# Kernel optimization log

Measured on AMD Instinct MI355X. Metric: run time of the kernel, lower is better.

The kernel has to match this reference:

```python
import jax, jax.numpy as jnp
import numpy as np

NUM_USERS = 100000
NUM_ITEMS = 20000
DIM = 64
NUM_TAG = 64
NUM_NEG = 8
B = 262144
M_IMP = 2000
MARGIN1 = 0.1
MARGIN2 = 0.1
LAMBDA1 = 1.0
LAMBDA2 = 1.0
TAU = 0.2
EPS = 1e-7
MAX_NORM = 1.0 - 1e-5


def _norm(x, keepdims=True):
    return jnp.sqrt(jnp.maximum(jnp.sum(x * x, -1, keepdims=keepdims), 1e-15))


def artanh(x):
    x = jnp.clip(x, -MAX_NORM, MAX_NORM)
    return 0.5 * (jnp.log1p(x) - jnp.log1p(-x))


def acosh(z):
    z = jnp.maximum(z, 1.0 + EPS)
    return jnp.log(z + jnp.sqrt(z * z - 1.0))


# ---- Poincare ball, c = 1 ----
def ball_projx(x):
    n = _norm(x)
    return jnp.where(n > MAX_NORM, x * (MAX_NORM / n), x)


def ball_expmap0(u):
    n = _norm(u)
    return jnp.tanh(n) * u / n


def ball_logmap0(x):
    n = _norm(x)
    return artanh(n) * x / n


def mobius_add(x, y):
    xy = jnp.sum(x * y, -1, keepdims=True)
    x2 = jnp.sum(x * x, -1, keepdims=True)
    y2 = jnp.sum(y * y, -1, keepdims=True)
    num = (1.0 + 2.0 * xy + y2) * x + (1.0 - x2) * y
    den = 1.0 + 2.0 * xy + x2 * y2
    return num / jnp.maximum(den, 1e-15)


def mobius_matvec(w, x):
    # x: [..., in], w: [out, in] -> mx = x @ w.T (geoopt convention)
    mx = x @ w.T
    xn = _norm(x)
    mn = _norm(mx)
    return jnp.tanh(mn / xn * artanh(xn)) * mx / mn


def ball_dist2(x, y):
    d = 2.0 * artanh(_norm(mobius_add(-x, y), keepdims=False))
    return d * d


# ---- Lorentz, k = 1 ----
def lorentz_dist2(x, y):
    inner = jnp.sum(x[..., 1:] * y[..., 1:], -1) - x[..., 0] * y[..., 0]
    d = acosh(-inner)
    return d * d


def setup_inputs() -> dict:
    key = jax.random.key(0)
    ks = jax.random.split(key, 10)
    # Lorentz points (k=1): x0 = sqrt(1 + ||x_spatial||^2)
    sp = jax.random.normal(ks[0], (NUM_USERS + NUM_ITEMS, DIM - 1), jnp.float32) * 0.5
    t = jnp.sqrt(1.0 + jnp.sum(sp * sp, -1, keepdims=True))
    embeddings = jnp.concatenate([t, sp], -1)
    vtg_weight = jax.random.normal(ks[1], (NUM_ITEMS, DIM), jnp.float32) * 0.01
    emb_tag = ball_expmap0(jax.random.normal(ks[2], (NUM_TAG, DIM), jnp.float32) * 0.1)
    kk = (6.0 / (2 * DIM)) ** 0.5
    lin_weight = jax.random.uniform(ks[3], (DIM, DIM), jnp.float32, -kk, kk)
    lin_bias = ball_expmap0(jax.random.normal(ks[4], (DIM,), jnp.float32) * 0.001)
    tag_weight = jnp.zeros((NUM_TAG,), jnp.float32)
    uu = jax.random.randint(ks[5], (B, 1), 0, NUM_USERS)
    it = jax.random.randint(ks[6], (B, 1 + NUM_NEG), NUM_USERS, NUM_USERS + NUM_ITEMS)
    triples = jnp.concatenate([uu, it], 1)
    tag_labels = jax.random.randint(ks[7], (NUM_ITEMS, NUM_TAG), 0, 2)
    a = jax.random.randint(ks[8], (M_IMP,), 0, NUM_TAG)
    b = (a + 1 + jax.random.randint(ks[9], (M_IMP,), 0, NUM_TAG - 1)) % NUM_TAG
    implication = jnp.stack([a, b], 1)
    return dict(embeddings=embeddings, vtg_weight=vtg_weight, emb_tag=emb_tag,
                lin_weight=lin_weight, lin_bias=lin_bias, tag_weight=tag_weight,
                triples=triples, tag_labels=tag_labels, implication=implication)


def reference(embeddings, vtg_weight, emb_tag, lin_weight, lin_bias, tag_weight,
              triples, tag_labels, implication):
    # ---- hyperbolic margin-ranking loss ----
    u = embeddings[triples[:, 0]]                         # [B, D]
    pos = embeddings[triples[:, 1]]                       # [B, D]
    neg = embeddings[triples[:, 2:]]                      # [B, NEG, D]
    pos_scores = lorentz_dist2(u, pos)[:, None]           # [B, 1]
    neg_scores = lorentz_dist2(u[:, None, :], neg)        # [B, NEG]
    # alpha = sqrt(dist2(u, origin)) = acosh(u0) for Lorentz k=1
    alpha = acosh(u[:, 0])[:, None]
    rank_loss = jnp.sum(jnp.maximum((pos_scores - neg_scores + MARGIN2) * alpha, 0.0))

    # ---- Ex_loss: MobiusLinear then tangent-space cdist ----
    enc = ball_projx(vtg_weight)
    h = mobius_matvec(lin_weight, enc)
    h = ball_projx(mobius_add(h, lin_bias[None, :]))
    a = ball_logmap0(h)                                   # [I, D]
    bt = ball_logmap0(emb_tag)                            # [T, D]
    sq = jnp.sum(a * a, -1)[:, None] + jnp.sum(bt * bt, -1)[None, :] - 2.0 * a @ bt.T
    dist = jnp.sqrt(jnp.maximum(sq, 1e-12))
    logits = dist / jnp.exp(tag_weight)[None, :]          # [I, T]
    logp = jnp.log(logits)
    # relu(log(target) - log(all_dist) + margin1) summed over all tags,
    # masked to the positive-tag positions (== np.where(tag_labels>0) gather)
    term = jnp.maximum(logp[:, :, None] - logp[:, None, :] + MARGIN1, 0.0)  # [I, T, T]
    mask = (tag_labels > 0).astype(logp.dtype)
    cls_loss = jnp.sum(term.sum(-1) * mask)

    # ---- tag-hierarchy contrastive loss ----
    q = emb_tag[implication[:, 0]]
    p = emb_tag[implication[:, 1]]
    dist_pos = ball_dist2(q, p)[:, None]                               # [M, 1]
    dist_neg = ball_dist2(q[:, None, :], emb_tag[None, :, :])          # [M, T]
    full = jnp.concatenate([dist_pos, dist_neg], 1)                    # [M, T+1]
    # original filters out entries <= 1e-9 (the self-distance zero); masking
    # them to -inf in logit space is the permutation-invariant equivalent
    cl_logits = jnp.where(full > 1e-9, -full / TAU, -1e30)
    cl_loss = jnp.sum(jax.nn.logsumexp(cl_logits, axis=1) + dist_pos[:, 0] / TAU)

    return rank_loss + LAMBDA1 * cls_loss + LAMBDA2 * cl_loss
```

## Files before the change

### kernel.cpp

```cpp
#include <hip/hip_runtime.h>
#include <math.h>

namespace {

constexpr int NUM_NEG   = 8;
constexpr int BROWS     = 262144;
constexpr int NUM_ITEMS_C = 20000;
constexpr int M_IMP_C   = 2000;
constexpr float MARGIN1 = 0.1f;
constexpr float MARGIN2 = 0.1f;
constexpr float TAU     = 0.2f;
constexpr float EPS1    = 1e-7f;
constexpr float MAXNORM = 1.0f - 1e-5f;

constexpr int NBLK   = 4096;
constexpr int NWAVES = NBLK * 4;

__device__ __forceinline__ float wredsum(float v) {
    v += __shfl_xor(v, 1);  v += __shfl_xor(v, 2);  v += __shfl_xor(v, 4);
    v += __shfl_xor(v, 8);  v += __shfl_xor(v, 16); v += __shfl_xor(v, 32);
    return v;
}
__device__ __forceinline__ float wredmax(float v) {
    v = fmaxf(v, __shfl_xor(v, 1));  v = fmaxf(v, __shfl_xor(v, 2));
    v = fmaxf(v, __shfl_xor(v, 4));  v = fmaxf(v, __shfl_xor(v, 8));
    v = fmaxf(v, __shfl_xor(v, 16)); v = fmaxf(v, __shfl_xor(v, 32));
    return v;
}
__device__ __forceinline__ float bcast(float v, int l) {
    return __int_as_float(__builtin_amdgcn_readlane(__float_as_int(v), l));
}
__device__ __forceinline__ float fsq(float x)  { return __builtin_amdgcn_sqrtf(x); }
__device__ __forceinline__ float frc(float x)  { return __builtin_amdgcn_rcpf(x); }
__device__ __forceinline__ float artanh_fast(float n) {
    n = fminf(n, MAXNORM);
    return 0.5f * __logf((1.f + n) * frc(1.f - n));
}
__device__ __forceinline__ float acosh_fast(float z) {
    z = fmaxf(z, 1.0f + EPS1);
    return __logf(z + fsq(fmaf(z, z, -1.0f)));
}
__device__ __forceinline__ float tanh_fast(float x) {
    const float t = __expf(2.f * x);
    return (t - 1.f) * frc(t + 1.f);
}
__device__ __forceinline__ float dot4(const float4& a, const float4& b) {
    return (a.x * b.x + a.y * b.y) + (a.z * b.z + a.w * b.w);
}

__global__ __launch_bounds__(256) void fused_kernel(
        const float* __restrict__ emb,  const int* __restrict__ tri,
        const float* __restrict__ vtg,  const float* __restrict__ etag,
        const float* __restrict__ linw, const float* __restrict__ linb,
        const float* __restrict__ tw,   const int* __restrict__ labels,
        const int* __restrict__ imp,    float* __restrict__ part) {
    __shared__ float SA[64 * 65];
    __shared__ float s64[64];
    __shared__ float red4[4];
    const int tid  = threadIdx.x;
    const int lane = tid & 63, wid = tid >> 6;
    const int b    = blockIdx.x;
    const int gw   = b * 4 + wid;
    float wacc = 0.f;

    for (int i = tid; i < 4096; i += 256) {
        const int r = i >> 6, d = i & 63;
        SA[d * 65 + r] = linw[i];
    }
    __syncthreads();
    const float bias = linb[lane];
    const float y2b  = wredsum(bias * bias);
    const int i0 = gw, i1 = gw + NWAVES;
    const bool v1 = (i1 < NUM_ITEMS_C);

    float xv0 = vtg[(long)i0 * 64 + lane];
    float xv1 = v1 ? vtg[(long)i1 * 64 + lane] : 0.f;

    auto prep = [&](float& x) -> float {
        float n2 = wredsum(x * x);
        float n  = fsq(fmaxf(n2, 1e-15f));
        if (n > MAXNORM) {
            x *= MAXNORM * frc(n);
            n2 = wredsum(x * x);
            n  = fsq(fmaxf(n2, 1e-15f));
        }
        return n;
    };
    const float xn0 = prep(xv0);
    const float xn1 = prep(xv1);

    float ma0 = 0.f, ma1 = 0.f, mb0 = 0.f, mb1 = 0.f;
    #pragma unroll
    for (int d = 0; d < 64; d += 2) {
        const float w0 = SA[(d)     * 65 + lane];
        const float w1 = SA[(d + 1) * 65 + lane];
        ma0 = fmaf(bcast(xv0, d), w0, ma0);  ma1 = fmaf(bcast(xv0, d + 1), w1, ma1);
        mb0 = fmaf(bcast(xv1, d), w0, mb0);  mb1 = fmaf(bcast(xv1, d + 1), w1, mb1);
    }
    auto tail = [&](float mx, float xn) -> float {
        const float mn  = fsq(fmaxf(wredsum(mx * mx), 1e-15f));
        const float g   = tanh_fast(mn * frc(xn) * artanh_fast(xn));
        const float h1  = g * frc(mn) * mx;
        const float x2h = wredsum(h1 * h1);
        const float xy  = wredsum(h1 * bias);
        const float A   = 1.f + 2.f * xy + y2b;
        const float Bc  = 1.f - x2h;
        const float den = fmaxf(1.f + 2.f * xy + x2h * y2b, 1e-15f);
        float hh = (A * h1 + Bc * bias) * frc(den);
        float hn = fsq(fmaxf(wredsum(hh * hh), 1e-15f));
        if (hn > MAXNORM) {
            hh *= MAXNORM * frc(hn);
            hn = fsq(fmaxf(wredsum(hh * hh), 1e-15f));
        }
        return artanh_fast(hn) * frc(hn) * hh;
    };
    const float av0 = tail(ma0 + ma1, xn0);
    const float av1 = tail(mb0 + mb1, xn1);
    __syncthreads();
    {
        const int j = tid >> 2, p = tid & 3;
        float e[16]; float s2 = 0.f;
        #pragma unroll
        for (int m = 0; m < 16; ++m) { e[m] = etag[j * 64 + p * 16 + m]; s2 += e[m] * e[m]; }
        s2 += __shfl_xor(s2, 1); s2 += __shfl_xor(s2, 2);
        const float n  = fsq(fmaxf(s2, 1e-15f));
        const float sc = artanh_fast(n) * frc(n);
        #pragma unroll
        for (int m = 0; m < 16; ++m) SA[(p * 16 + m) * 65 + j] = sc * e[m];
        if (p == 0) s64[j] = sc * sc * s2;
    }
    __syncthreads();
    const float twl = tw[lane];
    const float b2l = s64[lane];
    float da0 = 0.f, da1 = 0.f, db0 = 0.f, db1 = 0.f;
    #pragma unroll
    for (int d = 0; d < 64; d += 2) {
        const float w0 = SA[(d)     * 65 + lane];
        const float w1 = SA[(d + 1) * 65 + lane];
        da0 = fmaf(bcast(av0, d), w0, da0);  da1 = fmaf(bcast(av0, d + 1), w1, da1);
        db0 = fmaf(bcast(av1, d), w0, db0);  db1 = fmaf(bcast(av1, d + 1), w1, db1);
    }
    auto hinge = [&](float a, float dot, int i) -> float {
        const float a2v  = wredsum(a * a);
        const float dist = fsq(fmaxf(a2v + b2l - 2.f * dot, 1e-12f));
        const float logp = __logf(dist) - twl;
        float s0 = 0.f, s1 = 0.f, s2 = 0.f, s3 = 0.f;
        #pragma unroll
        for (int k = 0; k < 64; k += 4) {
            s0 += fmaxf(logp - bcast(logp, k)     + MARGIN1, 0.f);
            s1 += fmaxf(logp - bcast(logp, k + 1) + MARGIN1, 0.f);
            s2 += fmaxf(logp - bcast(logp, k + 2) + MARGIN1, 0.f);
            s3 += fmaxf(logp - bcast(logp, k + 3) + MARGIN1, 0.f);
        }
        const float hs = (s0 + s1) + (s2 + s3);
        const float c  = (labels[(long)i * 64 + lane] > 0) ? hs : 0.f;
        return wredsum(c);
    };
    wacc += hinge(av0, da0 + da1, i0);
    if (v1) wacc += hinge(av1, db0 + db1, i1);
    __syncthreads();

    {
        const int j = tid >> 2, p = tid & 3;
        float s2 = 0.f;
        #pragma unroll
        for (int m = 0; m < 16; ++m) {
            const float e = etag[j * 64 + p * 16 + m];
            s2 += e * e;
            SA[(p * 16 + m) * 65 + j] = e;
        }
        s2 += __shfl_xor(s2, 1); s2 += __shfl_xor(s2, 2);
        if (p == 0) s64[j] = s2;
    }
    __syncthreads();
    if (gw < M_IMP_C) {
        const int ai = imp[gw * 2];
        const int bi = imp[gw * 2 + 1];
        const float y2l = s64[lane];
        const float x2  = s64[ai];
        float c0 = 0.f, c1 = 0.f, c2 = 0.f, c3 = 0.f;
        #pragma unroll
        for (int d = 0; d < 64; d += 4) {
            c0 = fmaf(SA[(d)     * 65 + ai], SA[(d)     * 65 + lane], c0);
            c1 = fmaf(SA[(d + 1) * 65 + ai], SA[(d + 1) * 65 + lane], c1);
            c2 = fmaf(SA[(d + 2) * 65 + ai], SA[(d + 2) * 65 + lane], c2);
            c3 = fmaf(SA[(d + 3) * 65 + ai], SA[(d + 3) * 65 + lane], c3);
        }
        const float c   = (c0 + c1) + (c2 + c3);
        const float A   = 1.f - 2.f * c + y2l;
        const float Bc  = 1.f - x2;
        const float nn  = A * A * x2 - 2.f * A * Bc * c + Bc * Bc * y2l;
        const float den = fmaxf(1.f - 2.f * c + x2 * y2l, 1e-15f);
        float n = fsq(fmaxf(nn * frc(den * den), 1e-15f));
        n = fminf(n, MAXNORM);
        const float dd = __logf((1.f + n) * frc(1.f - n));
        float dist = dd * dd;
        if (lane == ai) dist = 0.f;
        const float logit = (dist > 1e-9f) ? (-dist * (1.f / TAU)) : -1e30f;
        const float dp = bcast(dist, bi);
        const float lp = bcast(logit, bi);
        const float m  = wredmax(logit);
        const float se = wredsum(__expf(logit - m)) + __expf(lp - m);
        wacc += m + __logf(se) + dp * (1.f / TAU);
    }

    {
        const int sub = lane & 7;
        const int rw  = lane >> 3;
        const int dof = sub * 8;
        const bool o0 = sub & 1;
        const bool o1 = (sub >> 1) & 1;
        const bool o2 = (sub >> 2) & 1;
        float racc = 0.f;

        const int  row0 = gw * 8 + rw;
        const int* t0 = tri + (long)row0 * 10;
        const int* t1 = t0 + (long)(NWAVES * 8) * 10;
        const int2 a01 = *reinterpret_cast<const int2*>(t0);
        const int2 a23 = *reinterpret_cast<const int2*>(t0 + 2);
        const int2 a45 = *reinterpret_cast<const int2*>(t0 + 4);
        const int2 a67 = *reinterpret_cast<const int2*>(t0 + 6);
        const int2 a89 = *reinterpret_cast<const int2*>(t0 + 8);
        const int2 b01 = *reinterpret_cast<const int2*>(t1);
        const int2 b23 = *reinterpret_cast<const int2*>(t1 + 2);
        const int2 b45 = *reinterpret_cast<const int2*>(t1 + 4);
        const int2 b67 = *reinterpret_cast<const int2*>(t1 + 6);
        const int2 b89 = *reinterpret_cast<const int2*>(t1 + 8);

        auto ldvec = [&](int idx, float4& lo, float4& hi) {
            const float* q = emb + (long)idx * 64 + dof;
            lo = *reinterpret_cast<const float4*>(q);
            hi = *reinterpret_cast<const float4*>(q + 4);
        };
        auto finish = [&](float e0, float e1, float e2, float e3,
                          float e4, float e5, float e6, float e7,
                          float ps, float alpha) {
            float s_;
            s_ = o0 ? e0 : e1; s_ = __shfl_xor(s_, 1); const float f0 = (o0 ? e1 : e0) + s_;
            s_ = o0 ? e2 : e3; s_ = __shfl_xor(s_, 1); const float f1 = (o0 ? e3 : e2) + s_;
            s_ = o0 ? e4 : e5; s_ = __shfl_xor(s_, 1); const float f2 = (o0 ? e5 : e4) + s_;
            s_ = o0 ? e6 : e7; s_ = __shfl_xor(s_, 1); const float f3 = (o0 ? e7 : e6) + s_;
            s_ = o1 ? f0 : f1; s_ = __shfl_xor(s_, 2); const float g0 = (o1 ? f1 : f0) + s_;
            s_ = o1 ? f2 : f3; s_ = __shfl_xor(s_, 2); const float g1 = (o1 ? f3 : f2) + s_;
            s_ = o2 ? g0 : g1; s_ = __shfl_xor(s_, 4); const float dn = (o2 ? g1 : g0) + s_;
            const float dneg = acosh_fast(-dn);
            float hk = fmaxf(ps - dneg * dneg + MARGIN2, 0.f);
            hk += __shfl_xor(hk, 1); hk += __shfl_xor(hk, 2); hk += __shfl_xor(hk, 4);
            if (sub == 0) racc += alpha * hk;
        };

        float4 ua0, ub0, pa0, pb0, ua1, ub1, pa1, pb1;
        ldvec(a01.x, ua0, ub0);  ldvec(a01.y, pa0, pb0);
        ldvec(b01.x, ua1, ub1);  ldvec(b01.y, pa1, pb1);

        float4 na0,nb0, na1,nb1, na2,nb2, na3,nb3, na4,nb4, na5,nb5, na6,nb6, na7,nb7;
        ldvec(a23.x, na0, nb0);  ldvec(a23.y, na1, nb1);
        ldvec(a45.x, na2, nb2);  ldvec(a45.y, na3, nb3);
        ldvec(a67.x, na4, nb4);  ldvec(a67.y, na5, nb5);
        ldvec(a89.x, na6, nb6);  ldvec(a89.y, na7, nb7);

        const float u00 = ua0.x;
        if (sub == 0) ua0.x = -ua0.x;
        float dp0 = dot4(ua0, pa0) + dot4(ub0, pb0);
        dp0 += __shfl_xor(dp0, 1); dp0 += __shfl_xor(dp0, 2); dp0 += __shfl_xor(dp0, 4);
        const float dpos0  = acosh_fast(-dp0);
        const float ps0    = dpos0 * dpos0;
        const float alpha0 = acosh_fast(u00);
        const float e0 = dot4(ua0, na0) + dot4(ub0, nb0);
        const float e1 = dot4(ua0, na1) + dot4(ub0, nb1);
        const float e2 = dot4(ua0, na2) + dot4(ub0, nb2);
        const float e3 = dot4(ua0, na3) + dot4(ub0, nb3);
        const float e4 = dot4(ua0, na4) + dot4(ub0, nb4);
        const float e5 = dot4(ua0, na5) + dot4(ub0, nb5);
        const float e6 = dot4(ua0, na6) + dot4(ub0, nb6);
        const float e7 = dot4(ua0, na7) + dot4(ub0, nb7);

        float4 ma0v,mb0v, ma1v,mb1v, ma2v,mb2v, ma3v,mb3v,
               ma4v,mb4v, ma5v,mb5v, ma6v,mb6v, ma7v,mb7v;
        ldvec(b23.x, ma0v, mb0v);  ldvec(b23.y, ma1v, mb1v);
        ldvec(b45.x, ma2v, mb2v);  ldvec(b45.y, ma3v, mb3v);
        ldvec(b67.x, ma4v, mb4v);  ldvec(b67.y, ma5v, mb5v);
        ldvec(b89.x, ma6v, mb6v);  ldvec(b89.y, ma7v, mb7v);

        finish(e0, e1, e2, e3, e4, e5, e6, e7, ps0, alpha0);

        const float u01 = ua1.x;
        if (sub == 0) ua1.x = -ua1.x;
        float dp1 = dot4(ua1, pa1) + dot4(ub1, pb1);
        dp1 += __shfl_xor(dp1, 1); dp1 += __shfl_xor(dp1, 2); dp1 += __shfl_xor(dp1, 4);
        const float dpos1  = acosh_fast(-dp1);
        const float ps1    = dpos1 * dpos1;
        const float alpha1 = acosh_fast(u01);
        const float h0 = dot4(ua1, ma0v) + dot4(ub1, mb0v);
        const float h1 = dot4(ua1, ma1v) + dot4(ub1, mb1v);
        const float h2 = dot4(ua1, ma2v) + dot4(ub1, mb2v);
        const float h3 = dot4(ua1, ma3v) + dot4(ub1, mb3v);
        const float h4 = dot4(ua1, ma4v) + dot4(ub1, mb4v);
        const float h5 = dot4(ua1, ma5v) + dot4(ub1, mb5v);
        const float h6 = dot4(ua1, ma6v) + dot4(ub1, mb6v);
        const float h7 = dot4(ua1, ma7v) + dot4(ub1, mb7v);
        finish(h0, h1, h2, h3, h4, h5, h6, h7, ps1, alpha1);

        wacc += wredsum(racc);
    }

    if (lane == 0) red4[wid] = wacc;
    __syncthreads();
    if (tid == 0) part[b] = red4[0] + red4[1] + red4[2] + red4[3];
}

__global__ __launch_bounds__(256) void final_reduce(
        const float* __restrict__ parts, int n, float* __restrict__ out) {
    __shared__ double red[256];
    double s = 0.0;
    for (int i = threadIdx.x; i < n; i += 256) s += (double)parts[i];
    red[threadIdx.x] = s;
    __syncthreads();
    for (int off = 128; off > 0; off >>= 1) {
        if (threadIdx.x < off) red[threadIdx.x] += red[threadIdx.x + off];
        __syncthreads();
    }
    if (threadIdx.x == 0) out[0] = (float)red[0];
}

}

extern "C" void kernel_launch(void* const* d_in, const int* in_sizes, int n_in,
                              void* d_out, int out_size, void* d_ws, size_t ws_size,
                              hipStream_t stream) {
    const float* emb    = (const float*)d_in[0];
    const float* vtg    = (const float*)d_in[1];
    const float* etag   = (const float*)d_in[2];
    const float* linw   = (const float*)d_in[3];
    const float* linb   = (const float*)d_in[4];
    const float* tw     = (const float*)d_in[5];
    const int*   tri    = (const int*)d_in[6];
    const int*   labels = (const int*)d_in[7];
    const int*   imp    = (const int*)d_in[8];
    float* parts = (float*)d_ws;

    fused_kernel<<<NBLK, 256, 0, stream>>>(emb, tri, vtg, etag, linw, linb,
                                           tw, labels, imp, parts);
    final_reduce<<<1, 256, 0, stream>>>(parts, NBLK, (float*)d_out);
}
```

Baseline: 84.06 us.

## Split fused loss kernel into separate rank, classification and contrastive kernels

The single fused kernel, where every block staged the linear weights and tag tables in shared memory and ran all three loss parts, is split into three kernels. Each kernel is sized to its own work: 4096 blocks for ranking, 2500 for classification (two items per wave, no bounds checks) and 500 for the contrastive loss. The ranking blocks no longer pay for the shared-memory setup and extra syncs of the other parts. The classification path now broadcasts through LDS instead of readlane and batches independent wave reductions. The cost is two extra kernel launches and the loss of overlap between the memory-bound ranking work and the compute-bound classification work.

```diff
diff --git a/kernel.cpp b/kernel.cpp
--- a/kernel.cpp
+++ b/kernel.cpp
@@ -5,7 +5,6 @@
 
 constexpr int NUM_NEG   = 8;
 constexpr int BROWS     = 262144;
-constexpr int NUM_ITEMS_C = 20000;
 constexpr int M_IMP_C   = 2000;
 constexpr float MARGIN1 = 0.1f;
 constexpr float MARGIN2 = 0.1f;
@@ -13,13 +12,39 @@
 constexpr float EPS1    = 1e-7f;
 constexpr float MAXNORM = 1.0f - 1e-5f;
 
-constexpr int NBLK   = 4096;
-constexpr int NWAVES = NBLK * 4;
+constexpr int RANK_BLOCKS = 4096;
+constexpr int RANK_WAVES  = RANK_BLOCKS * 4;
+constexpr int CLS_BLOCKS  = 2500;
+constexpr int CLS_WAVES   = CLS_BLOCKS * 4;
+constexpr int CL_BLOCKS   = 500;
+constexpr int NPART = RANK_BLOCKS + CLS_BLOCKS + CL_BLOCKS;
 
 __device__ __forceinline__ float wredsum(float v) {
     v += __shfl_xor(v, 1);  v += __shfl_xor(v, 2);  v += __shfl_xor(v, 4);
     v += __shfl_xor(v, 8);  v += __shfl_xor(v, 16); v += __shfl_xor(v, 32);
     return v;
+}
+__device__ __forceinline__ void wredsum2(float& a, float& b) {
+    a += __shfl_xor(a, 1);  b += __shfl_xor(b, 1);
+    a += __shfl_xor(a, 2);  b += __shfl_xor(b, 2);
+    a += __shfl_xor(a, 4);  b += __shfl_xor(b, 4);
+    a += __shfl_xor(a, 8);  b += __shfl_xor(b, 8);
+    a += __shfl_xor(a, 16); b += __shfl_xor(b, 16);
+    a += __shfl_xor(a, 32); b += __shfl_xor(b, 32);
+}
+__device__ __forceinline__ void wredsum4(float& a, float& b, float& c, float& d) {
+    a += __shfl_xor(a, 1);  b += __shfl_xor(b, 1);
+    c += __shfl_xor(c, 1);  d += __shfl_xor(d, 1);
+    a += __shfl_xor(a, 2);  b += __shfl_xor(b, 2);
+    c += __shfl_xor(c, 2);  d += __shfl_xor(d, 2);
+    a += __shfl_xor(a, 4);  b += __shfl_xor(b, 4);
+    c += __shfl_xor(c, 4);  d += __shfl_xor(d, 4);
+    a += __shfl_xor(a, 8);  b += __shfl_xor(b, 8);
+    c += __shfl_xor(c, 8);  d += __shfl_xor(d, 8);
+    a += __shfl_xor(a, 16); b += __shfl_xor(b, 16);
+    c += __shfl_xor(c, 16); d += __shfl_xor(d, 16);
+    a += __shfl_xor(a, 32); b += __shfl_xor(b, 32);
+    c += __shfl_xor(c, 32); d += __shfl_xor(d, 32);
 }
 __device__ __forceinline__ float wredmax(float v) {
     v = fmaxf(v, __shfl_xor(v, 1));  v = fmaxf(v, __shfl_xor(v, 2));
@@ -48,74 +73,183 @@
     return (a.x * b.x + a.y * b.y) + (a.z * b.z + a.w * b.w);
 }
 
-__global__ __launch_bounds__(256) void fused_kernel(
-        const float* __restrict__ emb,  const int* __restrict__ tri,
+__global__ __launch_bounds__(256) void rank_kernel(
+        const float* __restrict__ emb, const int* __restrict__ tri,
+        float* __restrict__ part) {
+    __shared__ float red4[4];
+    const int tid  = threadIdx.x;
+    const int lane = tid & 63, wid = tid >> 6;
+    const int gw   = blockIdx.x * 4 + wid;
+    const int sub  = lane & 7;
+    const int rw   = lane >> 3;
+    const int dof  = sub * 8;
+    const bool o0 = sub & 1;
+    const bool o1 = (sub >> 1) & 1;
+    const bool o2 = (sub >> 2) & 1;
+    float racc = 0.f;
+
+    const int  row0 = gw * 8 + rw;
+    const int* t0 = tri + (long)row0 * 10;
+    const int* t1 = t0 + (long)(RANK_WAVES * 8) * 10;
+    const int2 a01 = *reinterpret_cast<const int2*>(t0);
+    const int2 a23 = *reinterpret_cast<const int2*>(t0 + 2);
+    const int2 a45 = *reinterpret_cast<const int2*>(t0 + 4);
+    const int2 a67 = *reinterpret_cast<const int2*>(t0 + 6);
+    const int2 a89 = *reinterpret_cast<const int2*>(t0 + 8);
+    const int2 b01 = *reinterpret_cast<const int2*>(t1);
+    const int2 b23 = *reinterpret_cast<const int2*>(t1 + 2);
+    const int2 b45 = *reinterpret_cast<const int2*>(t1 + 4);
+    const int2 b67 = *reinterpret_cast<const int2*>(t1 + 6);
+    const int2 b89 = *reinterpret_cast<const int2*>(t1 + 8);
+
+    auto ldvec = [&](int idx, float4& lo, float4& hi) {
+        const float* q = emb + (long)idx * 64 + dof;
+        lo = *reinterpret_cast<const float4*>(q);
+        hi = *reinterpret_cast<const float4*>(q + 4);
+    };
+    auto finish = [&](float e0, float e1, float e2, float e3,
+                      float e4, float e5, float e6, float e7,
+                      float ps, float alpha) {
+        float s_;
+        s_ = o0 ? e0 : e1; s_ = __shfl_xor(s_, 1); const float f0 = (o0 ? e1 : e0) + s_;
+        s_ = o0 ? e2 : e3; s_ = __shfl_xor(s_, 1); const float f1 = (o0 ? e3 : e2) + s_;
+        s_ = o0 ? e4 : e5; s_ = __shfl_xor(s_, 1); const float f2 = (o0 ? e5 : e4) + s_;
+        s_ = o0 ? e6 : e7; s_ = __shfl_xor(s_, 1); const float f3 = (o0 ? e7 : e6) + s_;
+        s_ = o1 ? f0 : f1; s_ = __shfl_xor(s_, 2); const float g0 = (o1 ? f1 : f0) + s_;
+        s_ = o1 ? f2 : f3; s_ = __shfl_xor(s_, 2); const float g1 = (o1 ? f3 : f2) + s_;
+        s_ = o2 ? g0 : g1; s_ = __shfl_xor(s_, 4); const float dn = (o2 ? g1 : g0) + s_;
+        const float dneg = acosh_fast(-dn);
+        racc += alpha * fmaxf(ps - dneg * dneg + MARGIN2, 0.f);
+    };
+
+    float4 ua0, ub0, pa0, pb0, ua1, ub1, pa1, pb1;
+    ldvec(a01.x, ua0, ub0);  ldvec(a01.y, pa0, pb0);
+    ldvec(b01.x, ua1, ub1);  ldvec(b01.y, pa1, pb1);
+
+    float4 na0,nb0, na1,nb1, na2,nb2, na3,nb3, na4,nb4, na5,nb5, na6,nb6, na7,nb7;
+    ldvec(a23.x, na0, nb0);  ldvec(a23.y, na1, nb1);
+    ldvec(a45.x, na2, nb2);  ldvec(a45.y, na3, nb3);
+    ldvec(a67.x, na4, nb4);  ldvec(a67.y, na5, nb5);
+    ldvec(a89.x, na6, nb6);  ldvec(a89.y, na7, nb7);
+
+    const float u00 = ua0.x;
+    const float u0b0 = __shfl(u00, lane & 56);
+    if (sub == 0) ua0.x = -ua0.x;
+    float dp0 = dot4(ua0, pa0) + dot4(ub0, pb0);
+    dp0 += __shfl_xor(dp0, 1); dp0 += __shfl_xor(dp0, 2); dp0 += __shfl_xor(dp0, 4);
+    const float dpos0  = acosh_fast(-dp0);
+    const float ps0    = dpos0 * dpos0;
+    const float alpha0 = acosh_fast(u0b0);
+    const float e0 = dot4(ua0, na0) + dot4(ub0, nb0);
+    const float e1 = dot4(ua0, na1) + dot4(ub0, nb1);
+    const float e2 = dot4(ua0, na2) + dot4(ub0, nb2);
+    const float e3 = dot4(ua0, na3) + dot4(ub0, nb3);
+    const float e4 = dot4(ua0, na4) + dot4(ub0, nb4);
+    const float e5 = dot4(ua0, na5) + dot4(ub0, nb5);
+    const float e6 = dot4(ua0, na6) + dot4(ub0, nb6);
+    const float e7 = dot4(ua0, na7) + dot4(ub0, nb7);
+
+    float4 ma0v,mb0v, ma1v,mb1v, ma2v,mb2v, ma3v,mb3v,
+           ma4v,mb4v, ma5v,mb5v, ma6v,mb6v, ma7v,mb7v;
+    ldvec(b23.x, ma0v, mb0v);  ldvec(b23.y, ma1v, mb1v);
+    ldvec(b45.x, ma2v, mb2v);  ldvec(b45.y, ma3v, mb3v);
+    ldvec(b67.x, ma4v, mb4v);  ldvec(b67.y, ma5v, mb5v);
+    ldvec(b89.x, ma6v, mb6v);  ldvec(b89.y, ma7v, mb7v);
+
+    finish(e0, e1, e2, e3, e4, e5, e6, e7, ps0, alpha0);
+
+    const float u01 = ua1.x;
+    const float u0b1 = __shfl(u01, lane & 56);
+    if (sub == 0) ua1.x = -ua1.x;
+    float dp1 = dot4(ua1, pa1) + dot4(ub1, pb1);
+    dp1 += __shfl_xor(dp1, 1); dp1 += __shfl_xor(dp1, 2); dp1 += __shfl_xor(dp1, 4);
+    const float dpos1  = acosh_fast(-dp1);
+    const float ps1    = dpos1 * dpos1;
+    const float alpha1 = acosh_fast(u0b1);
+    const float h0 = dot4(ua1, ma0v) + dot4(ub1, mb0v);
+    const float h1 = dot4(ua1, ma1v) + dot4(ub1, mb1v);
+    const float h2 = dot4(ua1, ma2v) + dot4(ub1, mb2v);
+    const float h3 = dot4(ua1, ma3v) + dot4(ub1, mb3v);
+    const float h4 = dot4(ua1, ma4v) + dot4(ub1, mb4v);
+    const float h5 = dot4(ua1, ma5v) + dot4(ub1, mb5v);
+    const float h6 = dot4(ua1, ma6v) + dot4(ub1, mb6v);
+    const float h7 = dot4(ua1, ma7v) + dot4(ub1, mb7v);
+    finish(h0, h1, h2, h3, h4, h5, h6, h7, ps1, alpha1);
+
+    const float w = wredsum(racc);
+    if (lane == 0) red4[wid] = w;
+    __syncthreads();
+    if (tid == 0) part[blockIdx.x] = red4[0] + red4[1] + red4[2] + red4[3];
+}
+
+__global__ __launch_bounds__(256) void cls_kernel(
         const float* __restrict__ vtg,  const float* __restrict__ etag,
         const float* __restrict__ linw, const float* __restrict__ linb,
         const float* __restrict__ tw,   const int* __restrict__ labels,
-        const int* __restrict__ imp,    float* __restrict__ part) {
+        float* __restrict__ part) {
     __shared__ float SA[64 * 65];
-    __shared__ float s64[64];
+    __shared__ float XS[4 * 128];
+    __shared__ float s64v[64];
     __shared__ float red4[4];
     const int tid  = threadIdx.x;
     const int lane = tid & 63, wid = tid >> 6;
-    const int b    = blockIdx.x;
-    const int gw   = b * 4 + wid;
-    float wacc = 0.f;
+    const int gw   = blockIdx.x * 4 + wid;
+    const int i0   = gw, i1 = gw + CLS_WAVES;
+    const int xb   = wid * 128;
 
     for (int i = tid; i < 4096; i += 256) {
-        const int r = i >> 6, d = i & 63;
-        SA[d * 65 + r] = linw[i];
+        SA[(i & 63) * 65 + (i >> 6)] = linw[i];
     }
     __syncthreads();
     const float bias = linb[lane];
     const float y2b  = wredsum(bias * bias);
-    const int i0 = gw, i1 = gw + NWAVES;
-    const bool v1 = (i1 < NUM_ITEMS_C);
 
     float xv0 = vtg[(long)i0 * 64 + lane];
-    float xv1 = v1 ? vtg[(long)i1 * 64 + lane] : 0.f;
-
-    auto prep = [&](float& x) -> float {
-        float n2 = wredsum(x * x);
-        float n  = fsq(fmaxf(n2, 1e-15f));
-        if (n > MAXNORM) {
-            x *= MAXNORM * frc(n);
-            n2 = wredsum(x * x);
-            n  = fsq(fmaxf(n2, 1e-15f));
-        }
-        return n;
-    };
-    const float xn0 = prep(xv0);
-    const float xn1 = prep(xv1);
-
+    float xv1 = vtg[(long)i1 * 64 + lane];
+    float n20 = xv0 * xv0, n21 = xv1 * xv1;
+    wredsum2(n20, n21);
+    float xn0 = fsq(fmaxf(n20, 1e-15f)), xn1 = fsq(fmaxf(n21, 1e-15f));
+    if (xn0 > MAXNORM) { xv0 *= MAXNORM * frc(xn0); float t = wredsum(xv0 * xv0); xn0 = fsq(fmaxf(t, 1e-15f)); }
+    if (xn1 > MAXNORM) { xv1 *= MAXNORM * frc(xn1); float t = wredsum(xv1 * xv1); xn1 = fsq(fmaxf(t, 1e-15f)); }
+
+    XS[xb + lane]      = xv0;
+    XS[xb + 64 + lane] = xv1;
     float ma0 = 0.f, ma1 = 0.f, mb0 = 0.f, mb1 = 0.f;
     #pragma unroll
     for (int d = 0; d < 64; d += 2) {
         const float w0 = SA[(d)     * 65 + lane];
         const float w1 = SA[(d + 1) * 65 + lane];
-        ma0 = fmaf(bcast(xv0, d), w0, ma0);  ma1 = fmaf(bcast(xv0, d + 1), w1, ma1);
-        mb0 = fmaf(bcast(xv1, d), w0, mb0);  mb1 = fmaf(bcast(xv1, d + 1), w1, mb1);
-    }
-    auto tail = [&](float mx, float xn) -> float {
-        const float mn  = fsq(fmaxf(wredsum(mx * mx), 1e-15f));
-        const float g   = tanh_fast(mn * frc(xn) * artanh_fast(xn));
-        const float h1  = g * frc(mn) * mx;
-        const float x2h = wredsum(h1 * h1);
-        const float xy  = wredsum(h1 * bias);
-        const float A   = 1.f + 2.f * xy + y2b;
-        const float Bc  = 1.f - x2h;
-        const float den = fmaxf(1.f + 2.f * xy + x2h * y2b, 1e-15f);
-        float hh = (A * h1 + Bc * bias) * frc(den);
-        float hn = fsq(fmaxf(wredsum(hh * hh), 1e-15f));
-        if (hn > MAXNORM) {
-            hh *= MAXNORM * frc(hn);
-            hn = fsq(fmaxf(wredsum(hh * hh), 1e-15f));
-        }
-        return artanh_fast(hn) * frc(hn) * hh;
-    };
-    const float av0 = tail(ma0 + ma1, xn0);
-    const float av1 = tail(mb0 + mb1, xn1);
+        const float xA0 = XS[xb + d],      xA1 = XS[xb + d + 1];
+        const float xB0 = XS[xb + 64 + d], xB1 = XS[xb + 64 + d + 1];
+        ma0 = fmaf(xA0, w0, ma0);  ma1 = fmaf(xA1, w1, ma1);
+        mb0 = fmaf(xB0, w0, mb0);  mb1 = fmaf(xB1, w1, mb1);
+    }
+    const float mxA = ma0 + ma1, mxB = mb0 + mb1;
+
+    float mnA2 = mxA * mxA, mnB2 = mxB * mxB;
+    wredsum2(mnA2, mnB2);
+    const float mnA = fsq(fmaxf(mnA2, 1e-15f)), mnB = fsq(fmaxf(mnB2, 1e-15f));
+    const float gA = tanh_fast(mnA * frc(xn0) * artanh_fast(xn0));
+    const float gB = tanh_fast(mnB * frc(xn1) * artanh_fast(xn1));
+    const float hA = gA * frc(mnA) * mxA, hB = gB * frc(mnB) * mxB;
+    float x2hA = hA * hA, xyA = hA * bias, x2hB = hB * hB, xyB = hB * bias;
+    wredsum4(x2hA, xyA, x2hB, xyB);
+    const float AA  = 1.f + 2.f * xyA + y2b, AB = 1.f + 2.f * xyB + y2b;
+    const float BcA = 1.f - x2hA,            BcB = 1.f - x2hB;
+    const float denA = fmaxf(1.f + 2.f * xyA + x2hA * y2b, 1e-15f);
+    const float denB = fmaxf(1.f + 2.f * xyB + x2hB * y2b, 1e-15f);
+    float hhA = (AA * hA + BcA * bias) * frc(denA);
+    float hhB = (AB * hB + BcB * bias) * frc(denB);
+    float h2A = hhA * hhA, h2B = hhB * hhB;
+    wredsum2(h2A, h2B);
+    float hnA = fsq(fmaxf(h2A, 1e-15f)), hnB = fsq(fmaxf(h2B, 1e-15f));
+    if (hnA > MAXNORM) { hhA *= MAXNORM * frc(hnA); float t = wredsum(hhA * hhA); hnA = fsq(fmaxf(t, 1e-15f)); }
+    if (hnB > MAXNORM) { hhB *= MAXNORM * frc(hnB); float t = wredsum(hhB * hhB); hnB = fsq(fmaxf(t, 1e-15f)); }
+    const float aA = artanh_fast(hnA) * frc(hnA) * hhA;
+    const float aB = artanh_fast(hnB) * frc(hnB) * hhB;
+
+    XS[xb + lane]      = aA;
+    XS[xb + 64 + lane] = aB;
     __syncthreads();
     {
         const int j = tid >> 2, p = tid & 3;
@@ -127,39 +261,59 @@
         const float sc = artanh_fast(n) * frc(n);
         #pragma unroll
         for (int m = 0; m < 16; ++m) SA[(p * 16 + m) * 65 + j] = sc * e[m];
-        if (p == 0) s64[j] = sc * sc * s2;
-    }
-    __syncthreads();
-    const float twl = tw[lane];
-    const float b2l = s64[lane];
+        if (p == 0) s64v[j] = sc * sc * s2;
+    }
+    __syncthreads();
+
     float da0 = 0.f, da1 = 0.f, db0 = 0.f, db1 = 0.f;
     #pragma unroll
     for (int d = 0; d < 64; d += 2) {
         const float w0 = SA[(d)     * 65 + lane];
         const float w1 = SA[(d + 1) * 65 + lane];
-        da0 = fmaf(bcast(av0, d), w0, da0);  da1 = fmaf(bcast(av0, d + 1), w1, da1);
-        db0 = fmaf(bcast(av1, d), w0, db0);  db1 = fmaf(bcast(av1, d + 1), w1, db1);
-    }
-    auto hinge = [&](float a, float dot, int i) -> float {
-        const float a2v  = wredsum(a * a);
-        const float dist = fsq(fmaxf(a2v + b2l - 2.f * dot, 1e-12f));
-        const float logp = __logf(dist) - twl;
-        float s0 = 0.f, s1 = 0.f, s2 = 0.f, s3 = 0.f;
-        #pragma unroll
-        for (int k = 0; k < 64; k += 4) {
-            s0 += fmaxf(logp - bcast(logp, k)     + MARGIN1, 0.f);
-            s1 += fmaxf(logp - bcast(logp, k + 1) + MARGIN1, 0.f);
-            s2 += fmaxf(logp - bcast(logp, k + 2) + MARGIN1, 0.f);
-            s3 += fmaxf(logp - bcast(logp, k + 3) + MARGIN1, 0.f);
-        }
-        const float hs = (s0 + s1) + (s2 + s3);
-        const float c  = (labels[(long)i * 64 + lane] > 0) ? hs : 0.f;
-        return wredsum(c);
-    };
-    wacc += hinge(av0, da0 + da1, i0);
-    if (v1) wacc += hinge(av1, db0 + db1, i1);
-    __syncthreads();
-
+        const float xA0 = XS[xb + d],      xA1 = XS[xb + d + 1];
+        const float xB0 = XS[xb + 64 + d], xB1 = XS[xb + 64 + d + 1];
+        da0 = fmaf(xA0, w0, da0);  da1 = fmaf(xA1, w1, da1);
+        db0 = fmaf(xB0, w0, db0);  db1 = fmaf(xB1, w1, db1);
+    }
+    float a2A = aA * aA, a2B = aB * aB;
+    wredsum2(a2A, a2B);
+    const float b2l = s64v[lane];
+    const float twl = tw[lane];
+    const float distA = fsq(fmaxf(a2A + b2l - 2.f * (da0 + da1), 1e-12f));
+    const float distB = fsq(fmaxf(a2B + b2l - 2.f * (db0 + db1), 1e-12f));
+    const float lpA = __logf(distA) - twl;
+    const float lpB = __logf(distB) - twl;
+
+    XS[xb + lane]      = lpA;
+    XS[xb + 64 + lane] = lpB;
+    const float qA = lpA + MARGIN1, qB = lpB + MARGIN1;
+    float s00 = 0.f, s01 = 0.f, s10 = 0.f, s11 = 0.f;
+    #pragma unroll
+    for (int k = 0; k < 64; k += 2) {
+        const float lA0 = XS[xb + k],      lA1 = XS[xb + k + 1];
+        const float lB0 = XS[xb + 64 + k], lB1 = XS[xb + 64 + k + 1];
+        s00 += fmaxf(qA - lA0, 0.f);  s01 += fmaxf(qA - lA1, 0.f);
+        s10 += fmaxf(qB - lB0, 0.f);  s11 += fmaxf(qB - lB1, 0.f);
+    }
+    const float hsA = s00 + s01, hsB = s10 + s11;
+    const float cA = (labels[(long)i0 * 64 + lane] > 0) ? hsA : 0.f;
+    const float cB = (labels[(long)i1 * 64 + lane] > 0) ? hsB : 0.f;
+    const float w = wredsum(cA + cB);
+
+    if (lane == 0) red4[wid] = w;
+    __syncthreads();
+    if (tid == 0) part[blockIdx.x] = red4[0] + red4[1] + red4[2] + red4[3];
+}
+
+__global__ __launch_bounds__(256) void cl_kernel(
+        const float* __restrict__ etag, const int* __restrict__ imp,
+        float* __restrict__ part) {
+    __shared__ float SA[64 * 65];
+    __shared__ float s64v[64];
+    __shared__ float red4[4];
+    const int tid  = threadIdx.x;
+    const int lane = tid & 63, wid = tid >> 6;
+    const int gw   = blockIdx.x * 4 + wid;
     {
         const int j = tid >> 2, p = tid & 3;
         float s2 = 0.f;
@@ -170,143 +324,41 @@
             SA[(p * 16 + m) * 65 + j] = e;
         }
         s2 += __shfl_xor(s2, 1); s2 += __shfl_xor(s2, 2);
-        if (p == 0) s64[j] = s2;
-    }
-    __syncthreads();
-    if (gw < M_IMP_C) {
-        const int ai = imp[gw * 2];
-        const int bi = imp[gw * 2 + 1];
-        const float y2l = s64[lane];
-        const float x2  = s64[ai];
-        float c0 = 0.f, c1 = 0.f, c2 = 0.f, c3 = 0.f;
-        #pragma unroll
-        for (int d = 0; d < 64; d += 4) {
-            c0 = fmaf(SA[(d)     * 65 + ai], SA[(d)     * 65 + lane], c0);
-            c1 = fmaf(SA[(d + 1) * 65 + ai], SA[(d + 1) * 65 + lane], c1);
-            c2 = fmaf(SA[(d + 2) * 65 + ai], SA[(d + 2) * 65 + lane], c2);
-            c3 = fmaf(SA[(d + 3) * 65 + ai], SA[(d + 3) * 65 + lane], c3);
-        }
-        const float c   = (c0 + c1) + (c2 + c3);
-        const float A   = 1.f - 2.f * c + y2l;
-        const float Bc  = 1.f - x2;
-        const float nn  = A * A * x2 - 2.f * A * Bc * c + Bc * Bc * y2l;
-        const float den = fmaxf(1.f - 2.f * c + x2 * y2l, 1e-15f);
-        float n = fsq(fmaxf(nn * frc(den * den), 1e-15f));
-        n = fminf(n, MAXNORM);
-        const float dd = __logf((1.f + n) * frc(1.f - n));
-        float dist = dd * dd;
-        if (lane == ai) dist = 0.f;
-        const float logit = (dist > 1e-9f) ? (-dist * (1.f / TAU)) : -1e30f;
-        const float dp = bcast(dist, bi);
-        const float lp = bcast(logit, bi);
-        const float m  = wredmax(logit);
-        const float se = wredsum(__expf(logit - m)) + __expf(lp - m);
-        wacc += m + __logf(se) + dp * (1.f / TAU);
-    }
-
-    {
-        const int sub = lane & 7;
-        const int rw  = lane >> 3;
-        const int dof = sub * 8;
-        const bool o0 = sub & 1;
-        const bool o1 = (sub >> 1) & 1;
-        const bool o2 = (sub >> 2) & 1;
-        float racc = 0.f;
-
-        const int  row0 = gw * 8 + rw;
-        const int* t0 = tri + (long)row0 * 10;
-        const int* t1 = t0 + (long)(NWAVES * 8) * 10;
-        const int2 a01 = *reinterpret_cast<const int2*>(t0);
-        const int2 a23 = *reinterpret_cast<const int2*>(t0 + 2);
-        const int2 a45 = *reinterpret_cast<const int2*>(t0 + 4);
-        const int2 a67 = *reinterpret_cast<const int2*>(t0 + 6);
-        const int2 a89 = *reinterpret_cast<const int2*>(t0 + 8);
-        const int2 b01 = *reinterpret_cast<const int2*>(t1);
-        const int2 b23 = *reinterpret_cast<const int2*>(t1 + 2);
-        const int2 b45 = *reinterpret_cast<const int2*>(t1 + 4);
-        const int2 b67 = *reinterpret_cast<const int2*>(t1 + 6);
-        const int2 b89 = *reinterpret_cast<const int2*>(t1 + 8);
-
-        auto ldvec = [&](int idx, float4& lo, float4& hi) {
-            const float* q = emb + (long)idx * 64 + dof;
-            lo = *reinterpret_cast<const float4*>(q);
-            hi = *reinterpret_cast<const float4*>(q + 4);
-        };
-        auto finish = [&](float e0, float e1, float e2, float e3,
-                          float e4, float e5, float e6, float e7,
-                          float ps, float alpha) {
-            float s_;
-            s_ = o0 ? e0 : e1; s_ = __shfl_xor(s_, 1); const float f0 = (o0 ? e1 : e0) + s_;
-            s_ = o0 ? e2 : e3; s_ = __shfl_xor(s_, 1); const float f1 = (o0 ? e3 : e2) + s_;
-            s_ = o0 ? e4 : e5; s_ = __shfl_xor(s_, 1); const float f2 = (o0 ? e5 : e4) + s_;
-            s_ = o0 ? e6 : e7; s_ = __shfl_xor(s_, 1); const float f3 = (o0 ? e7 : e6) + s_;
-            s_ = o1 ? f0 : f1; s_ = __shfl_xor(s_, 2); const float g0 = (o1 ? f1 : f0) + s_;
-            s_ = o1 ? f2 : f3; s_ = __shfl_xor(s_, 2); const float g1 = (o1 ? f3 : f2) + s_;
-            s_ = o2 ? g0 : g1; s_ = __shfl_xor(s_, 4); const float dn = (o2 ? g1 : g0) + s_;
-            const float dneg = acosh_fast(-dn);
-            float hk = fmaxf(ps - dneg * dneg + MARGIN2, 0.f);
-            hk += __shfl_xor(hk, 1); hk += __shfl_xor(hk, 2); hk += __shfl_xor(hk, 4);
-            if (sub == 0) racc += alpha * hk;
-        };
-
-        float4 ua0, ub0, pa0, pb0, ua1, ub1, pa1, pb1;
-        ldvec(a01.x, ua0, ub0);  ldvec(a01.y, pa0, pb0);
-        ldvec(b01.x, ua1, ub1);  ldvec(b01.y, pa1, pb1);
-
-        float4 na0,nb0, na1,nb1, na2,nb2, na3,nb3, na4,nb4, na5,nb5, na6,nb6, na7,nb7;
-        ldvec(a23.x, na0, nb0);  ldvec(a23.y, na1, nb1);
-        ldvec(a45.x, na2, nb2);  ldvec(a45.y, na3, nb3);
-        ldvec(a67.x, na4, nb4);  ldvec(a67.y, na5, nb5);
-        ldvec(a89.x, na6, nb6);  ldvec(a89.y, na7, nb7);
-
-        const float u00 = ua0.x;
-        if (sub == 0) ua0.x = -ua0.x;
-        float dp0 = dot4(ua0, pa0) + dot4(ub0, pb0);
-        dp0 += __shfl_xor(dp0, 1); dp0 += __shfl_xor(dp0, 2); dp0 += __shfl_xor(dp0, 4);
-        const float dpos0  = acosh_fast(-dp0);
-        const float ps0    = dpos0 * dpos0;
-        const float alpha0 = acosh_fast(u00);
-        const float e0 = dot4(ua0, na0) + dot4(ub0, nb0);
-        const float e1 = dot4(ua0, na1) + dot4(ub0, nb1);
-        const float e2 = dot4(ua0, na2) + dot4(ub0, nb2);
-        const float e3 = dot4(ua0, na3) + dot4(ub0, nb3);
-        const float e4 = dot4(ua0, na4) + dot4(ub0, nb4);
-        const float e5 = dot4(ua0, na5) + dot4(ub0, nb5);
-        const float e6 = dot4(ua0, na6) + dot4(ub0, nb6);
-        const float e7 = dot4(ua0, na7) + dot4(ub0, nb7);
-
-        float4 ma0v,mb0v, ma1v,mb1v, ma2v,mb2v, ma3v,mb3v,
-               ma4v,mb4v, ma5v,mb5v, ma6v,mb6v, ma7v,mb7v;
-        ldvec(b23.x, ma0v, mb0v);  ldvec(b23.y, ma1v, mb1v);
-        ldvec(b45.x, ma2v, mb2v);  ldvec(b45.y, ma3v, mb3v);
-        ldvec(b67.x, ma4v, mb4v);  ldvec(b67.y, ma5v, mb5v);
-        ldvec(b89.x, ma6v, mb6v);  ldvec(b89.y, ma7v, mb7v);
-
-        finish(e0, e1, e2, e3, e4, e5, e6, e7, ps0, alpha0);
-
-        const float u01 = ua1.x;
-        if (sub == 0) ua1.x = -ua1.x;
-        float dp1 = dot4(ua1, pa1) + dot4(ub1, pb1);
-        dp1 += __shfl_xor(dp1, 1); dp1 += __shfl_xor(dp1, 2); dp1 += __shfl_xor(dp1, 4);
-        const float dpos1  = acosh_fast(-dp1);
-        const float ps1    = dpos1 * dpos1;
-        const float alpha1 = acosh_fast(u01);
-        const float h0 = dot4(ua1, ma0v) + dot4(ub1, mb0v);
-        const float h1 = dot4(ua1, ma1v) + dot4(ub1, mb1v);
-        const float h2 = dot4(ua1, ma2v) + dot4(ub1, mb2v);
-        const float h3 = dot4(ua1, ma3v) + dot4(ub1, mb3v);
-        const float h4 = dot4(ua1, ma4v) + dot4(ub1, mb4v);
-        const float h5 = dot4(ua1, ma5v) + dot4(ub1, mb5v);
-        const float h6 = dot4(ua1, ma6v) + dot4(ub1, mb6v);
-        const float h7 = dot4(ua1, ma7v) + dot4(ub1, mb7v);
-        finish(h0, h1, h2, h3, h4, h5, h6, h7, ps1, alpha1);
-
-        wacc += wredsum(racc);
-    }
-
-    if (lane == 0) red4[wid] = wacc;
-    __syncthreads();
-    if (tid == 0) part[b] = red4[0] + red4[1] + red4[2] + red4[3];
+        if (p == 0) s64v[j] = s2;
+    }
+    __syncthreads();
+    const int ai = imp[gw * 2];
+    const int bi = imp[gw * 2 + 1];
+    const float y2l = s64v[lane];
+    const float x2  = s64v[ai];
+    float c0 = 0.f, c1 = 0.f, c2 = 0.f, c3 = 0.f;
+    #pragma unroll
+    for (int d = 0; d < 64; d += 4) {
+        c0 = fmaf(SA[(d)     * 65 + ai], SA[(d)     * 65 + lane], c0);
+        c1 = fmaf(SA[(d + 1) * 65 + ai], SA[(d + 1) * 65 + lane], c1);
+        c2 = fmaf(SA[(d + 2) * 65 + ai], SA[(d + 2) * 65 + lane], c2);
+        c3 = fmaf(SA[(d + 3) * 65 + ai], SA[(d + 3) * 65 + lane], c3);
+    }
+    const float c   = (c0 + c1) + (c2 + c3);
+    const float A   = 1.f - 2.f * c + y2l;
+    const float Bc  = 1.f - x2;
+    const float nn  = A * A * x2 - 2.f * A * Bc * c + Bc * Bc * y2l;
+    const float den = fmaxf(1.f - 2.f * c + x2 * y2l, 1e-15f);
+    float n = fsq(fmaxf(nn * frc(den * den), 1e-15f));
+    n = fminf(n, MAXNORM);
+    const float dd = __logf((1.f + n) * frc(1.f - n));
+    float dist = dd * dd;
+    if (lane == ai) dist = 0.f;
+    const float logit = (dist > 1e-9f) ? (-dist * (1.f / TAU)) : -1e30f;
+    const float dp = bcast(dist, bi);
+    const float lp = bcast(logit, bi);
+    const float m  = wredmax(logit);
+    const float se = wredsum(__expf(logit - m)) + __expf(lp - m);
+    const float w  = m + __logf(se) + dp * (1.f / TAU);
+
+    if (lane == 0) red4[wid] = w;
+    __syncthreads();
+    if (tid == 0) part[blockIdx.x] = red4[0] + red4[1] + red4[2] + red4[3];
 }
 
 __global__ __launch_bounds__(256) void final_reduce(
@@ -339,7 +391,10 @@
     const int*   imp    = (const int*)d_in[8];
     float* parts = (float*)d_ws;
 
-    fused_kernel<<<NBLK, 256, 0, stream>>>(emb, tri, vtg, etag, linw, linb,
-                                           tw, labels, imp, parts);
-    final_reduce<<<1, 256, 0, stream>>>(parts, NBLK, (float*)d_out);
-}
+    rank_kernel<<<RANK_BLOCKS, 256, 0, stream>>>(emb, tri, parts);
+    cls_kernel<<<CLS_BLOCKS, 256, 0, stream>>>(vtg, etag, linw, linb, tw, labels,
+                                               parts + RANK_BLOCKS);
+    cl_kernel<<<CL_BLOCKS, 256, 0, stream>>>(etag, imp,
+                                             parts + RANK_BLOCKS + CLS_BLOCKS);
+    final_reduce<<<1, 256, 0, stream>>>(parts, NPART, (float*)d_out);
+}
```

New measurement: 96.42 us. +14.7%, slower.
